# Optimization experiments

Measured on AMD Instinct MI355X. Metric: run time of the kernel, lower is better.

The kernel has to match this reference:

```python
import jax, jax.numpy as jnp
import numpy as np

B, S, D = 2, 2048, 3584
H, KV, HD = 28, 4, 128
N_REP = H // KV          # 7
MAX_S = 2048
SCALE = HD ** -0.5
ROPE_BASE = 1_000_000.0  # Qwen2 rope theta


def _rope_tables(max_s, hd, base):
    inv = 1.0 / (base ** (np.arange(0, hd, 2, dtype=np.float32) / hd))  # [hd/2]
    ang = np.arange(max_s, dtype=np.float32)[:, None] * inv[None, :]    # [S, hd/2]
    return jnp.asarray(np.cos(ang)), jnp.asarray(np.sin(ang))


def apply_rotary(x, cos, sin):
    # x: [b, s, h, hd] with interleaved complex pairs (torch view_as_complex layout)
    xr = x[..., 0::2]
    xi = x[..., 1::2]
    cos = cos[None, :, None, :]
    sin = sin[None, :, None, :]
    yr = xr * cos - xi * sin
    yi = xr * sin + xi * cos
    return jnp.stack([yr, yi], axis=-1).reshape(x.shape)


def setup_inputs() -> dict:
    key = jax.random.key(0)
    ks = jax.random.split(key, 8)
    w = 0.02
    x = jax.random.normal(ks[0], (B, S, D), jnp.float32)
    wq_w = jax.random.normal(ks[1], (H * HD, D), jnp.float32) * w
    wq_b = jax.random.normal(ks[2], (H * HD,), jnp.float32) * w
    wk_w = jax.random.normal(ks[3], (KV * HD, D), jnp.float32) * w
    wk_b = jax.random.normal(ks[4], (KV * HD,), jnp.float32) * w
    wv_w = jax.random.normal(ks[5], (KV * HD, D), jnp.float32) * w
    wv_b = jax.random.normal(ks[6], (KV * HD,), jnp.float32) * w
    wo_w = jax.random.normal(ks[7], (D, H * HD), jnp.float32) * w
    k_cache = jnp.zeros((B, MAX_S, KV, HD), jnp.float32)
    v_cache = jnp.zeros((B, MAX_S, KV, HD), jnp.float32)
    freqs_cos, freqs_sin = _rope_tables(MAX_S, HD, ROPE_BASE)
    # causal additive mask [s, t]; large-negative instead of -inf for safe grads
    mask = jnp.triu(jnp.full((S, S), -1e9, jnp.float32), k=1)
    return {"x": x, "wq_w": wq_w, "wq_b": wq_b, "wk_w": wk_w, "wk_b": wk_b,
            "wv_w": wv_w, "wv_b": wv_b, "wo_w": wo_w,
            "k_cache": k_cache, "v_cache": v_cache,
            "freqs_cos": freqs_cos, "freqs_sin": freqs_sin,
            "mask": mask, "start_pos": 0}


def reference(x, wq_w, wq_b, wk_w, wk_b, wv_w, wv_b, wo_w,
              k_cache, v_cache, freqs_cos, freqs_sin, mask, start_pos):
    bsz, seqlen, _ = x.shape
    end_pos = start_pos + seqlen
    q = (x @ wq_w.T + wq_b).reshape(bsz, seqlen, H, HD)
    k = (x @ wk_w.T + wk_b).reshape(bsz, seqlen, KV, HD)
    v = (x @ wv_w.T + wv_b).reshape(bsz, seqlen, KV, HD)
    cos = jax.lax.dynamic_slice_in_dim(freqs_cos, start_pos, seqlen, 0)
    sin = jax.lax.dynamic_slice_in_dim(freqs_sin, start_pos, seqlen, 0)
    q = apply_rotary(q, cos, sin)
    k = apply_rotary(k, cos, sin)
    # KV-cache write
    k_cache = jax.lax.dynamic_update_slice(k_cache, k, (0, start_pos, 0, 0))
    v_cache = jax.lax.dynamic_update_slice(v_cache, v, (0, start_pos, 0, 0))
    keys = k_cache[:bsz, :end_pos]    # [b, t, kv, hd]
    values = v_cache[:bsz, :end_pos]
    # GQA: repeat_interleave kv heads to n_heads
    keys = jnp.repeat(keys, N_REP, axis=2)      # [b, t, h, hd]
    values = jnp.repeat(values, N_REP, axis=2)
    scores = jnp.einsum('bshd,bthd->bsht', q, keys) * SCALE
    scores = scores + mask[None, :, None, :]
    probs = jax.nn.softmax(scores.astype(jnp.float32), axis=-1).astype(x.dtype)
    out = jnp.einsum('bsht,bthd->bshd', probs, values)
    out = out.reshape(bsz, seqlen, H * HD)
    return out @ wo_w.T
```

## Files before the change

### kernel.cpp

```cpp
#include <hip/hip_runtime.h>
#include <hip/hip_bf16.h>

typedef __attribute__((ext_vector_type(4)))  float  f32x4;
typedef __attribute__((ext_vector_type(16))) float  f32x16;
typedef __attribute__((ext_vector_type(8)))  __bf16 bf16x8;
typedef __attribute__((ext_vector_type(4)))  __bf16 bf16x4;
typedef __attribute__((ext_vector_type(4)))  unsigned int u32x4;

constexpr int S_LEN = 2048, DMODEL = 3584, NH = 28, NKV = 4, HD = 128, NREP = 7;
constexpr float SCALE_LOG2 = 0.1275174331f;

__device__ __forceinline__ unsigned int pack2(float a, float b) {
  unsigned short ua = __builtin_bit_cast(unsigned short, (__bf16)a);
  unsigned short ub = __builtin_bit_cast(unsigned short, (__bf16)b);
  return (unsigned int)ua | ((unsigned int)ub << 16);
}

__global__ void cvt5_kernel(const float* __restrict__ s0, const float* __restrict__ s1,
                            const float* __restrict__ s2, const float* __restrict__ s3,
                            const float* __restrict__ s4,
                            __bf16* __restrict__ d0, __bf16* __restrict__ d1,
                            __bf16* __restrict__ d2, __bf16* __restrict__ d3,
                            __bf16* __restrict__ d4,
                            int n0, int n1, int n2, int n3, int* __restrict__ ctr, int total) {
  if (blockIdx.x == 0 && threadIdx.x == 0) *ctr = 0;
  for (int i = blockIdx.x * blockDim.x + threadIdx.x; i < total; i += gridDim.x * blockDim.x) {
    const float* s; __bf16* d; int j = i;
    if (j < n0) { s = s0; d = d0; }
    else { j -= n0;
      if (j < n1) { s = s1; d = d1; }
      else { j -= n1;
        if (j < n2) { s = s2; d = d2; }
        else { j -= n2;
          if (j < n3) { s = s3; d = d3; }
          else { j -= n3; s = s4; d = d4; }
        }
      }
    }
    float4 v = reinterpret_cast<const float4*>(s)[j];
    bf16x4 o;
    o[0] = (__bf16)v.x; o[1] = (__bf16)v.y; o[2] = (__bf16)v.z; o[3] = (__bf16)v.w;
    reinterpret_cast<bf16x4*>(d)[j] = o;
  }
}

#define GLDS16(gsrc, ldst)                                                              \
  __builtin_amdgcn_global_load_lds((const __attribute__((address_space(1))) void*)(gsrc),\
                                   (__attribute__((address_space(3))) void*)(ldst), 16, 0, 0)

template <int MODE>
__global__ __launch_bounds__(512, 2) void gemm256(
    const __bf16* __restrict__ A, const __bf16* __restrict__ Bw,
    const float* __restrict__ bias, void* __restrict__ Cout,
    int M, int N, int K,
    const float* __restrict__ fcos, const float* __restrict__ fsin,
    const int* __restrict__ sp_ptr, float scale)
{
  extern __shared__ char smem[];
  const int tid = threadIdx.x;
  const int lane = tid & 63, wid = tid >> 6;
  const int wm = wid >> 2, wn = wid & 3;
  const int l15 = lane & 15, g = (lane >> 4) & 3;

  const int chunk = gridDim.x >> 3;
  const int wg = (blockIdx.x & 7) * chunk + (blockIdx.x >> 3);
  const int nbx = N >> 8;
  const int by = wg / nbx, bx = wg % nbx;
  const int row0 = by * 256, col0 = bx * 256;

  const int srL   = 16 * (tid >> 6) + ((tid >> 2) & 15);
  const int cperm = ((tid & 3) * 8) ^ (((tid >> 5) & 1) * 16);
  const __bf16* pA0 = A + (size_t)(row0 + srL) * K + cperm;
  const __bf16* pA1 = pA0 + (size_t)128 * K;
  const __bf16* pB0 = Bw + (size_t)(col0 + srL) * K + cperm;
  const __bf16* pB1 = pB0 + (size_t)128 * K;
  char* ldsA = smem + tid * 16;
  char* ldsB = smem + 65536 + tid * 16;

  const int sw = ((l15 >> 3) & 1) << 5;
  const int aoff = wm * 8192 + l15 * 64 + ((g * 16) ^ sw);
  const int boff = 65536 + wn * 4096 + l15 * 64 + ((g * 16) ^ sw);

  f32x4 acc[8][4] = {};
  const int nt = K >> 5;

#pragma unroll
  for (int pt = 0; pt < 3; pt++) {
    const size_t ko = (size_t)pt * 32;
    char* sA = ldsA + pt * 16384;
    char* sB = ldsB + pt * 16384;
    GLDS16(pA0 + ko, sA);
    GLDS16(pA1 + ko, sA + 8192);
    GLDS16(pB0 + ko, sB);
    GLDS16(pB1 + ko, sB + 8192);
  }
  asm volatile("s_waitcnt vmcnt(8)" ::: "memory");
  __builtin_amdgcn_s_barrier();
  __builtin_amdgcn_sched_barrier(0);

  for (int t = 0; t < nt; t++) {
    const int slot = (t & 3) * 16384;
    const char* sa = smem + slot + aoff;
    const char* sb = smem + slot + boff;
    bf16x8 a0[4], a1[4], bfv[4];

#pragma unroll
    for (int fn = 0; fn < 4; fn++)
      bfv[fn] = *reinterpret_cast<const bf16x8*>(sb + fn * 1024);
#pragma unroll
    for (int fm = 0; fm < 4; fm++)
      a0[fm] = *reinterpret_cast<const bf16x8*>(sa + fm * 1024);
#pragma unroll
    for (int fm = 0; fm < 4; fm++)
      a1[fm] = *reinterpret_cast<const bf16x8*>(sa + (4 + fm) * 1024);

    if (t + 3 < nt) {
      const size_t ko = (size_t)(t + 3) * 32;
      char* sA = ldsA + ((t + 3) & 3) * 16384;
      char* sB = ldsB + ((t + 3) & 3) * 16384;
      GLDS16(pA0 + ko, sA);
      GLDS16(pA1 + ko, sA + 8192);
      GLDS16(pB0 + ko, sB);
      GLDS16(pB1 + ko, sB + 8192);
    }

    asm volatile("s_waitcnt lgkmcnt(4)" ::: "memory");
    __builtin_amdgcn_sched_barrier(0);
    __builtin_amdgcn_s_setprio(1);
#pragma unroll
    for (int fn = 0; fn < 4; fn++)
#pragma unroll
      for (int fm = 0; fm < 4; fm++)
        acc[fm][fn] = __builtin_amdgcn_mfma_f32_16x16x32_bf16(a0[fm], bfv[fn], acc[fm][fn], 0, 0, 0);
    __builtin_amdgcn_s_setprio(0);

    asm volatile("s_waitcnt lgkmcnt(0)" ::: "memory");
    __builtin_amdgcn_sched_barrier(0);
    __builtin_amdgcn_s_setprio(1);
#pragma unroll
    for (int fn = 0; fn < 4; fn++)
#pragma unroll
      for (int fm = 0; fm < 4; fm++)
        acc[4 + fm][fn] = __builtin_amdgcn_mfma_f32_16x16x32_bf16(a1[fm], bfv[fn], acc[4 + fm][fn], 0, 0, 0);
    __builtin_amdgcn_s_setprio(0);

    if (t < nt - 3)       asm volatile("s_waitcnt vmcnt(8)" ::: "memory");
    else if (t == nt - 3) asm volatile("s_waitcnt vmcnt(4)" ::: "memory");
    else if (t == nt - 2) asm volatile("s_waitcnt vmcnt(0)" ::: "memory");
    __builtin_amdgcn_s_barrier();
    __builtin_amdgcn_sched_barrier(0);
  }

  if constexpr (MODE == 0) {
    float* C = (float*)Cout;
#pragma unroll
    for (int fm = 0; fm < 8; fm++) {
      const int row = row0 + wm * 128 + fm * 16 + 4 * g;
#pragma unroll
      for (int fn = 0; fn < 4; fn++) {
        const int col = col0 + wn * 64 + fn * 16 + l15;
#pragma unroll
        for (int r = 0; r < 4; r++)
          C[(size_t)(row + r) * N + col] = acc[fm][fn][r];
      }
    }
  } else {
    __bf16* C = (__bf16*)Cout;
    const int sp = sp_ptr[0];
    float bval[4];
#pragma unroll
    for (int fn = 0; fn < 4; fn++) bval[fn] = bias[col0 + wn * 64 + fn * 16 + l15];
#pragma unroll
    for (int fm = 0; fm < 8; fm++) {
#pragma unroll
      for (int fn = 0; fn < 4; fn++) {
        const int col = col0 + wn * 64 + fn * 16 + l15;
        const int i = (col & (HD - 1)) >> 1;
#pragma unroll
        for (int r = 0; r < 4; r++) {
          const int row = row0 + wm * 128 + fm * 16 + 4 * g + r;
          float y = acc[fm][fn][r] + bval[fn];
          float p = __shfl_xor(y, 1);
          const int spos = sp + (row & (S_LEN - 1));
          const float c = fcos[spos * (HD / 2) + i];
          const float sn = fsin[spos * (HD / 2) + i];
          y = (col & 1) ? (p * sn + y * c) : (y * c - p * sn);
          C[(size_t)row * N + col] = (__bf16)(y * scale);
        }
      }
    }
  }
}

__global__ __launch_bounds__(256) void gemm_kv(
    const __bf16* __restrict__ A,
    const __bf16* __restrict__ Wk, const float* __restrict__ bk, __bf16* __restrict__ Ko,
    const __bf16* __restrict__ Wv, const float* __restrict__ bv, __bf16* __restrict__ Vo,
    const float* __restrict__ fcos, const float* __restrict__ fsin,
    const int* __restrict__ sp_ptr)
{
  constexpr int N = 512, K = 3584;
  __shared__ __bf16 As[128 * 32];
  __shared__ __bf16 Bs[128 * 32];
  const int tid = threadIdx.x;
  const int lane = tid & 63, wid = tid >> 6;
  const int l15 = lane & 15, g = lane >> 4;
  const int wr = wid >> 1, wc = wid & 1;
  const bool isK = blockIdx.x < 4;
  const __bf16* Bw = isK ? Wk : Wv;
  const float* bias = isK ? bk : bv;
  __bf16* Cout = isK ? Ko : Vo;
  const int row0 = blockIdx.y * 128;
  const int col0 = (blockIdx.x & 3) * 128;

  f32x4 acc[4][4] = {};

  const int srow = tid >> 2;
  const int scol = (tid & 3) * 8;
  const __bf16* Ag0 = A + (size_t)(row0 + srow) * K + scol;
  const __bf16* Ag1 = Ag0 + (size_t)64 * K;
  const __bf16* Bg0 = Bw + (size_t)(col0 + srow) * K + scol;
  const __bf16* Bg1 = Bg0 + (size_t)64 * K;
  __bf16* As0 = As + tid * 8;
  __bf16* As1 = As + 2048 + tid * 8;
  __bf16* Bs0 = Bs + tid * 8;
  __bf16* Bs1 = Bs + 2048 + tid * 8;

  for (int k0 = 0; k0 < K; k0 += 32) {
    GLDS16(Ag0 + k0, As0);
    GLDS16(Ag1 + k0, As1);
    GLDS16(Bg0 + k0, Bs0);
    GLDS16(Bg1 + k0, Bs1);
    __syncthreads();
    bf16x8 af[4], bfr[4];
#pragma unroll
    for (int m = 0; m < 4; m++)
      af[m] = *reinterpret_cast<const bf16x8*>(As + (wr * 64 + m * 16 + l15) * 32 + g * 8);
#pragma unroll
    for (int n = 0; n < 4; n++)
      bfr[n] = *reinterpret_cast<const bf16x8*>(Bs + (wc * 64 + n * 16 + l15) * 32 + g * 8);
#pragma unroll
    for (int m = 0; m < 4; m++)
#pragma unroll
      for (int n = 0; n < 4; n++)
        acc[m][n] = __builtin_amdgcn_mfma_f32_16x16x32_bf16(af[m], bfr[n], acc[m][n], 0, 0, 0);
    __syncthreads();
  }

  const int sp = sp_ptr[0];
#pragma unroll
  for (int m = 0; m < 4; m++) {
#pragma unroll
    for (int n = 0; n < 4; n++) {
      const int col = col0 + wc * 64 + n * 16 + l15;
      const float bval = bias[col];
      f32x4 v = acc[m][n];
#pragma unroll
      for (int r = 0; r < 4; r++) {
        const int row = row0 + wr * 64 + m * 16 + 4 * g + r;
        float y = v[r] + bval;
        if (isK) {
          float p = __shfl_xor(y, 1);
          const int i = (col & (HD - 1)) >> 1;
          const int spos = sp + (row & (S_LEN - 1));
          const float c = fcos[spos * (HD / 2) + i];
          const float sn = fsin[spos * (HD / 2) + i];
          y = (col & 1) ? (p * sn + y * c) : (y * c - p * sn);
        }
        Cout[(size_t)row * N + col] = (__bf16)y;
      }
    }
  }
}

__global__ void vtrans_kernel(const __bf16* __restrict__ Vg, __bf16* __restrict__ Vt) {
  __shared__ __bf16 t[32][33];
  const int bkv = blockIdx.z;
  const int b = bkv >> 2, kv = bkv & 3;
  const int s0 = blockIdx.x * 32, h0 = blockIdx.y * 32;
  const int tid = threadIdx.x;
#pragma unroll
  for (int c = 0; c < 4; c++) {
    int idx = c * 256 + tid;
    int sr = idx >> 5, hc = idx & 31;
    t[sr][hc] = Vg[(((size_t)b * S_LEN + s0 + sr) * NKV + kv) * HD + h0 + hc];
  }
  __syncthreads();
#pragma unroll
  for (int c = 0; c < 4; c++) {
    int idx = c * 256 + tid;
    int hr = idx >> 5, sc = idx & 31;
    Vt[(((size_t)b * NKV + kv) * HD + h0 + hr) * S_LEN + s0 + sc] = t[sc][hr];
  }
}

__global__ __launch_bounds__(256, 2) void attn_kernel(
    const __bf16* __restrict__ Qb, const __bf16* __restrict__ Kb,
    const __bf16* __restrict__ Vt, __bf16* __restrict__ Ob, int* __restrict__ ctr)
{
  __shared__ __align__(16) char asmem[65536];
  __shared__ int jsh;

  const int tid = threadIdx.x, lane = tid & 63, wid = tid >> 6;
  const int l31 = lane & 31, hh = lane >> 5;

  const int trow = tid >> 4;
  const int kcol = (((tid & 15) * 16) ^ ((trow & 7) << 4)) >> 1;
  const int vrow = tid >> 3;
  const int vcol = (((tid & 7) * 16) ^ ((vrow & 7) << 4)) >> 1;

  constexpr int NITEMS = 16 * NH * 2;

  while (true) {
    if (tid == 0) jsh = atomicAdd(ctr, 1);
    __syncthreads();
    const int j = jsh;
    if (j >= NITEMS) break;

    const int qi = 15 - (j / 56);
    const int r56 = j % 56;
    const int h = r56 >> 1, b = r56 & 1;
    const int kvh = h / NREP;
    const int qw = qi * 128 + wid * 32;
    const int qg = qw + l31;

    const __bf16* Kbase = Kb + ((size_t)b * S_LEN * NKV + kvh) * HD;
    const __bf16* Vbase = Vt + ((size_t)b * NKV + kvh) * (size_t)HD * S_LEN;

    bf16x8 qf[8];
    {
      const __bf16* qp = Qb + (((size_t)b * S_LEN + qg) * NH + h) * HD + hh * 8;
#pragma unroll
      for (int c = 0; c < 8; c++) qf[c] = *reinterpret_cast<const bf16x8*>(qp + c * 16);
    }

    f32x16 o[4] = {};
    float mrun = -3.0e38f, lsum = 0.0f;

    const int ntiles = 2 * qi + 2;

#define STAGE(T, S)                                                                     \
    do {                                                                                \
      const int k0_ = (T) * 64;                                                         \
      char* Kd_ = asmem + (S) * 32768;                                                  \
      char* Vd_ = Kd_ + 16384;                                                          \
      _Pragma("unroll")                                                                 \
      for (int p = 0; p < 4; p++) {                                                     \
        GLDS16(Kbase + (size_t)(k0_ + p * 16 + trow) * (NKV * HD) + kcol,               \
               Kd_ + (p * 256 + tid) * 16);                                             \
        GLDS16(Vbase + (size_t)(p * 32 + vrow) * S_LEN + k0_ + vcol,                    \
               Vd_ + (p * 256 + tid) * 16);                                             \
      }                                                                                 \
    } while (0)

    STAGE(0, 0);

    for (int t = 0; t < ntiles; t++) {
      __syncthreads();
      if (t + 1 < ntiles) STAGE(t + 1, (t + 1) & 1);

      const char* Ksb = asmem + (t & 1) * 32768;
      const char* Vsb = Ksb + 16384;
      const int k0 = t * 64;

      f32x16 s0 = {}, s1 = {};
      {
        const char* kp0 = Ksb + l31 * 256;
        const char* kp1 = kp0 + 32 * 256;
        const int sw = (l31 & 7) << 4;
        __builtin_amdgcn_s_setprio(1);
#pragma unroll
        for (int c = 0; c < 8; c++) {
          const int cb = (c * 32 + hh * 16) ^ sw;
          bf16x8 kf0 = *reinterpret_cast<const bf16x8*>(kp0 + cb);
          s0 = __builtin_amdgcn_mfma_f32_32x32x16_bf16(kf0, qf[c], s0, 0, 0, 0);
          bf16x8 kf1 = *reinterpret_cast<const bf16x8*>(kp1 + cb);
          s1 = __builtin_amdgcn_mfma_f32_32x32x16_bf16(kf1, qf[c], s1, 0, 0, 0);
        }
        __builtin_amdgcn_s_setprio(0);
      }

      if (k0 + 63 > qw) {
#pragma unroll
        for (int r = 0; r < 16; r++) {
          const int kvo = k0 + ((r & 3) + 8 * (r >> 2)) + 4 * hh;
          if (kvo > qg)      s0[r] = -1.0e9f;
          if (kvo + 32 > qg) s1[r] = -1.0e9f;
        }
      }

      float pmax = -3.0e38f;
#pragma unroll
      for (int r = 0; r < 16; r++) { pmax = fmaxf(pmax, s0[r]); pmax = fmaxf(pmax, s1[r]); }
      pmax = fmaxf(pmax, __shfl_xor(pmax, 32));
      if (!__all(pmax <= mrun + 11.5f)) {
        const float mnew = fmaxf(mrun, pmax);
        const float fs = exp2f(mrun - mnew);
        lsum *= fs;
#pragma unroll
        for (int dt = 0; dt < 4; dt++) o[dt] *= fs;
        mrun = mnew;
      }
      float psum = 0.0f;
#pragma unroll
      for (int r = 0; r < 16; r++) {
        s0[r] = exp2f(s0[r] - mrun); psum += s0[r];
        s1[r] = exp2f(s1[r] - mrun); psum += s1[r];
      }
      lsum += psum;

      unsigned int pk[2][8], px[2][8];
#pragma unroll
      for (int jj = 0; jj < 8; jj++) {
        pk[0][jj] = pack2(s0[2 * jj], s0[2 * jj + 1]);
        pk[1][jj] = pack2(s1[2 * jj], s1[2 * jj + 1]);
      }
#pragma unroll
      for (int tt = 0; tt < 2; tt++)
#pragma unroll
        for (int jj = 0; jj < 8; jj++) px[tt][jj] = __shfl_xor(pk[tt][jj], 32);

      __builtin_amdgcn_s_setprio(1);
#pragma unroll
      for (int tt = 0; tt < 2; tt++) {
#pragma unroll
        for (int c2 = 0; c2 < 2; c2++) {
          u32x4 pb4;
          if (hh == 0)
            pb4 = (u32x4){pk[tt][4 * c2], pk[tt][4 * c2 + 1], px[tt][4 * c2], px[tt][4 * c2 + 1]};
          else
            pb4 = (u32x4){px[tt][4 * c2 + 2], px[tt][4 * c2 + 3], pk[tt][4 * c2 + 2], pk[tt][4 * c2 + 3]};
          bf16x8 pbf = __builtin_bit_cast(bf16x8, pb4);
          const int colb = tt * 64 + c2 * 32 + hh * 16;
#pragma unroll
          for (int dt = 0; dt < 4; dt++) {
            const int d = dt * 32 + l31;
            bf16x8 vf = *reinterpret_cast<const bf16x8*>(Vsb + d * 128 + (colb ^ ((d & 7) << 4)));
            o[dt] = __builtin_amdgcn_mfma_f32_32x32x16_bf16(vf, pbf, o[dt], 0, 0, 0);
          }
        }
      }
      __builtin_amdgcn_s_setprio(0);
    }
#undef STAGE

    lsum += __shfl_xor(lsum, 32);
    const float inv = 1.0f / lsum;
    char* my = asmem + wid * 8192;
#pragma unroll
    for (int dt = 0; dt < 4; dt++) {
#pragma unroll
      for (int jj = 0; jj < 8; jj++) {
        const int r = 2 * jj;
        const int d = dt * 32 + ((r & 3) + 8 * (r >> 2)) + 4 * hh;
        const unsigned int w = pack2(o[dt][r] * inv, o[dt][r + 1] * inv);
        *reinterpret_cast<unsigned int*>(my + ((l31 * 256 + d * 2) ^ ((l31 & 7) << 4))) = w;
      }
    }
#pragma unroll
    for (int jj = 0; jj < 8; jj++) {
      const int idx = jj * 64 + lane;
      const int row = idx >> 4, c16 = idx & 15;
      u32x4 val = *reinterpret_cast<u32x4*>(my + row * 256 + ((c16 * 16) ^ ((row & 7) << 4)));
      *reinterpret_cast<u32x4*>(Ob + (size_t)(b * S_LEN + qw + row) * (NH * HD) + h * HD + c16 * 8) = val;
    }
  }
}

extern "C" void kernel_launch(void* const* d_in, const int* in_sizes, int n_in,
                              void* d_out, int out_size, void* d_ws, size_t ws_size,
                              hipStream_t stream) {
  (void)in_sizes; (void)n_in; (void)out_size; (void)ws_size;
  const float* x    = (const float*)d_in[0];
  const float* wq_w = (const float*)d_in[1];
  const float* wq_b = (const float*)d_in[2];
  const float* wk_w = (const float*)d_in[3];
  const float* wk_b = (const float*)d_in[4];
  const float* wv_w = (const float*)d_in[5];
  const float* wv_b = (const float*)d_in[6];
  const float* wo_w = (const float*)d_in[7];
  const float* fcos = (const float*)d_in[10];
  const float* fsin = (const float*)d_in[11];
  const int*   spp  = (const int*)d_in[13];
  float* out = (float*)d_out;

  constexpr size_t XB_N = (size_t)4096 * 3584;
  constexpr size_t WQ_N = (size_t)3584 * 3584;
  constexpr size_t WK_N = (size_t)512 * 3584;
  constexpr size_t WO_N = (size_t)3584 * 3584;
  constexpr size_t KB_N = (size_t)4096 * 512;

  __bf16* xb  = (__bf16*)d_ws;
  __bf16* wqb = xb + XB_N;
  __bf16* wkb = wqb + WQ_N;
  __bf16* wvb = wkb + WK_N;
  __bf16* wob = wvb + WK_N;
  __bf16* Qb  = wob + WO_N;
  __bf16* Kb  = Qb + XB_N;
  __bf16* Vg  = Kb + KB_N;
  __bf16* Vt  = Vg + KB_N;
  int*    ctr = (int*)(Vt + KB_N);
  __bf16* Ob  = xb;

  constexpr int N0 = (int)(XB_N / 4), N1 = (int)(WQ_N / 4), N2 = (int)(WK_N / 4),
                N3 = (int)(WK_N / 4), N4 = (int)(WO_N / 4);
  constexpr int NTOT = N0 + N1 + N2 + N3 + N4;
  cvt5_kernel<<<2048, 256, 0, stream>>>(x, wq_w, wk_w, wv_w, wo_w,
                                        xb, wqb, wkb, wvb, wob,
                                        N0, N1, N2, N3, ctr, NTOT);

  gemm256<2><<<dim3(224), 512, 131072, stream>>>(xb, wqb, wq_b, Qb, 4096, 3584, 3584,
                                                 fcos, fsin, spp, SCALE_LOG2);
  gemm_kv<<<dim3(8, 32), 256, 0, stream>>>(xb, wkb, wk_b, Kb, wvb, wv_b, Vg,
                                           fcos, fsin, spp);
  vtrans_kernel<<<dim3(64, 4, 8), 256, 0, stream>>>(Vg, Vt);
  attn_kernel<<<dim3(512), 256, 0, stream>>>(Qb, Kb, Vt, Ob, ctr);
  gemm256<0><<<dim3(224), 512, 131072, stream>>>(Ob, wob, nullptr, out, 4096, 3584, 3584,
                                                 nullptr, nullptr, nullptr, 1.0f);
}
```

Baseline: 432.9 us.

## Restructure GEMM main loop into double-buffered 64-wide K tiles with phased loads

Replaces the 4-slot, 3-deep prefetch ring of 32-wide K tiles with a two-buffer scheme over 64-wide K tiles. Each iteration is split into four MFMA phases, and global-to-LDS loads for the next tile are interleaved between them. Barriers are placed around each MFMA phase in a ping-pong style. The aim is better overlap of loads with MFMA work and fewer loop iterations, at the cost of more barriers per iteration and a shallower prefetch distance.

```diff
diff --git a/kernel.cpp b/kernel.cpp
--- a/kernel.cpp
+++ b/kernel.cpp
@@ -74,82 +74,85 @@
   const __bf16* pA1 = pA0 + (size_t)128 * K;
   const __bf16* pB0 = Bw + (size_t)(col0 + srL) * K + cperm;
   const __bf16* pB1 = pB0 + (size_t)128 * K;
-  char* ldsA = smem + tid * 16;
-  char* ldsB = smem + 65536 + tid * 16;
-
-  const int sw = ((l15 >> 3) & 1) << 5;
-  const int aoff = wm * 8192 + l15 * 64 + ((g * 16) ^ sw);
-  const int boff = 65536 + wn * 4096 + l15 * 64 + ((g * 16) ^ sw);
+  char* lds = smem + tid * 16;
+
+  const int rdo = l15 * 64 + ((g * 16) ^ (((l15 >> 3) & 1) << 5));
+  const int abase = wm * 8192 + rdo;
+  const int bbase = 32768 + (wn >> 1) * 8192 + (wn & 1) * 4096 + rdo;
 
   f32x4 acc[8][4] = {};
-  const int nt = K >> 5;
-
-#pragma unroll
-  for (int pt = 0; pt < 3; pt++) {
-    const size_t ko = (size_t)pt * 32;
-    char* sA = ldsA + pt * 16384;
-    char* sB = ldsB + pt * 16384;
-    GLDS16(pA0 + ko, sA);
-    GLDS16(pA1 + ko, sA + 8192);
-    GLDS16(pB0 + ko, sB);
-    GLDS16(pB1 + ko, sB + 8192);
-  }
-  asm volatile("s_waitcnt vmcnt(8)" ::: "memory");
+  const int nt = K >> 6;
+
+  GLDS16(pA0,      lds);          GLDS16(pA1,      lds + 8192);
+  GLDS16(pB0,      lds + 32768);  GLDS16(pB1,      lds + 40960);
+  GLDS16(pA0 + 32, lds + 16384);  GLDS16(pA1 + 32, lds + 24576);
+  GLDS16(pB0 + 32, lds + 49152);  GLDS16(pB1 + 32, lds + 57344);
+  asm volatile("s_waitcnt vmcnt(4)" ::: "memory");
   __builtin_amdgcn_s_barrier();
   __builtin_amdgcn_sched_barrier(0);
 
+#define PHASE_MFMA(ACCROW)                                                              \
+  __builtin_amdgcn_s_barrier();                                                         \
+  asm volatile("s_waitcnt lgkmcnt(0)" ::: "memory");                                    \
+  __builtin_amdgcn_sched_barrier(0);                                                    \
+  __builtin_amdgcn_s_setprio(1);                                                        \
+  _Pragma("unroll")                                                                     \
+  for (int fn = 0; fn < 4; fn++)                                                        \
+    _Pragma("unroll")                                                                   \
+    for (int fm = 0; fm < 4; fm++)                                                      \
+      acc[ACCROW + fm][fn] =                                                            \
+          __builtin_amdgcn_mfma_f32_16x16x32_bf16(af[fm], bfv[fn], acc[ACCROW + fm][fn],\
+                                                  0, 0, 0);                             \
+  __builtin_amdgcn_s_setprio(0);                                                        \
+  __builtin_amdgcn_s_barrier();
+
   for (int t = 0; t < nt; t++) {
-    const int slot = (t & 3) * 16384;
-    const char* sa = smem + slot + aoff;
-    const char* sb = smem + slot + boff;
-    bf16x8 a0[4], a1[4], bfv[4];
+    const int bb = (t & 1) << 16;
+    const char* sab = smem + bb;
+    char* stg = lds + (((t + 1) & 1) << 16);
+    const bool st = (t + 1 < nt);
+    const size_t ko = (size_t)(t + 1) * 64;
+    bf16x8 af[4], bfv[4];
 
 #pragma unroll
     for (int fn = 0; fn < 4; fn++)
-      bfv[fn] = *reinterpret_cast<const bf16x8*>(sb + fn * 1024);
+      bfv[fn] = *reinterpret_cast<const bf16x8*>(sab + bbase + fn * 1024);
 #pragma unroll
     for (int fm = 0; fm < 4; fm++)
-      a0[fm] = *reinterpret_cast<const bf16x8*>(sa + fm * 1024);
+      af[fm] = *reinterpret_cast<const bf16x8*>(sab + abase + fm * 1024);
+    if (st) { GLDS16(pA0 + ko, stg); GLDS16(pA1 + ko, stg + 8192); }
+    PHASE_MFMA(0)
+
 #pragma unroll
     for (int fm = 0; fm < 4; fm++)
-      a1[fm] = *reinterpret_cast<const bf16x8*>(sa + (4 + fm) * 1024);
-
-    if (t + 3 < nt) {
-      const size_t ko = (size_t)(t + 3) * 32;
-      char* sA = ldsA + ((t + 3) & 3) * 16384;
-      char* sB = ldsB + ((t + 3) & 3) * 16384;
-      GLDS16(pA0 + ko, sA);
-      GLDS16(pA1 + ko, sA + 8192);
-      GLDS16(pB0 + ko, sB);
-      GLDS16(pB1 + ko, sB + 8192);
-    }
-
-    asm volatile("s_waitcnt lgkmcnt(4)" ::: "memory");
-    __builtin_amdgcn_sched_barrier(0);
-    __builtin_amdgcn_s_setprio(1);
+      af[fm] = *reinterpret_cast<const bf16x8*>(sab + abase + (4 + fm) * 1024);
+    if (st) {
+      GLDS16(pB0 + ko, stg + 32768); GLDS16(pB1 + ko, stg + 40960);
+      asm volatile("s_waitcnt vmcnt(4)" ::: "memory");
+    } else {
+      asm volatile("s_waitcnt vmcnt(0)" ::: "memory");
+    }
+    PHASE_MFMA(4)
+
 #pragma unroll
     for (int fn = 0; fn < 4; fn++)
-#pragma unroll
-      for (int fm = 0; fm < 4; fm++)
-        acc[fm][fn] = __builtin_amdgcn_mfma_f32_16x16x32_bf16(a0[fm], bfv[fn], acc[fm][fn], 0, 0, 0);
-    __builtin_amdgcn_s_setprio(0);
-
-    asm volatile("s_waitcnt lgkmcnt(0)" ::: "memory");
-    __builtin_amdgcn_sched_barrier(0);
-    __builtin_amdgcn_s_setprio(1);
-#pragma unroll
-    for (int fn = 0; fn < 4; fn++)
-#pragma unroll
-      for (int fm = 0; fm < 4; fm++)
-        acc[4 + fm][fn] = __builtin_amdgcn_mfma_f32_16x16x32_bf16(a1[fm], bfv[fn], acc[4 + fm][fn], 0, 0, 0);
-    __builtin_amdgcn_s_setprio(0);
-
-    if (t < nt - 3)       asm volatile("s_waitcnt vmcnt(8)" ::: "memory");
-    else if (t == nt - 3) asm volatile("s_waitcnt vmcnt(4)" ::: "memory");
-    else if (t == nt - 2) asm volatile("s_waitcnt vmcnt(0)" ::: "memory");
-    __builtin_amdgcn_s_barrier();
-    __builtin_amdgcn_sched_barrier(0);
-  }
+      bfv[fn] = *reinterpret_cast<const bf16x8*>(sab + bbase + 16384 + fn * 1024);
+#pragma unroll
+    for (int fm = 0; fm < 4; fm++)
+      af[fm] = *reinterpret_cast<const bf16x8*>(sab + abase + 16384 + fm * 1024);
+    if (st) { GLDS16(pA0 + ko + 32, stg + 16384); GLDS16(pA1 + ko + 32, stg + 24576); }
+    PHASE_MFMA(0)
+
+#pragma unroll
+    for (int fm = 0; fm < 4; fm++)
+      af[fm] = *reinterpret_cast<const bf16x8*>(sab + abase + 16384 + (4 + fm) * 1024);
+    if (st) {
+      GLDS16(pB0 + ko + 32, stg + 49152); GLDS16(pB1 + ko + 32, stg + 57344);
+      asm volatile("s_waitcnt vmcnt(4)" ::: "memory");
+    }
+    PHASE_MFMA(4)
+  }
+#undef PHASE_MFMA
 
   if constexpr (MODE == 0) {
     float* C = (float*)Cout;
```

After: 440.4 us. Within noise of the previous version (+1.7%).

## Fuse V transpose into KV GEMM, use static attention grid with single-buffered LDS

Applied to the files above, without the earlier changes.

The V projection epilogue now writes directly into the transposed [b,kv,d,s] layout, removing the separate transpose kernel and its intermediate buffer. The attention kernel drops the atomic work-queue persistent loop and launches one block per work item (896) in a snake-ordered mapping to balance causal work. LDS is halved to a single K/V stage so four blocks can share a CU, giving up double-buffered prefetch in favour of occupancy. The V epilogue stores 4-element strided chunks, which may be less coalesced.

```diff
diff --git a/kernel.cpp b/kernel.cpp
--- a/kernel.cpp
+++ b/kernel.cpp
@@ -22,8 +22,7 @@
                             __bf16* __restrict__ d0, __bf16* __restrict__ d1,
                             __bf16* __restrict__ d2, __bf16* __restrict__ d3,
                             __bf16* __restrict__ d4,
-                            int n0, int n1, int n2, int n3, int* __restrict__ ctr, int total) {
-  if (blockIdx.x == 0 && threadIdx.x == 0) *ctr = 0;
+                            int n0, int n1, int n2, int n3, int total) {
   for (int i = blockIdx.x * blockDim.x + threadIdx.x; i < total; i += gridDim.x * blockDim.x) {
     const float* s; __bf16* d; int j = i;
     if (j < n0) { s = s0; d = d0; }
@@ -195,7 +194,7 @@
 __global__ __launch_bounds__(256) void gemm_kv(
     const __bf16* __restrict__ A,
     const __bf16* __restrict__ Wk, const float* __restrict__ bk, __bf16* __restrict__ Ko,
-    const __bf16* __restrict__ Wv, const float* __restrict__ bv, __bf16* __restrict__ Vo,
+    const __bf16* __restrict__ Wv, const float* __restrict__ bv, __bf16* __restrict__ Vt,
     const float* __restrict__ fcos, const float* __restrict__ fsin,
     const int* __restrict__ sp_ptr)
 {
@@ -209,7 +208,6 @@
   const bool isK = blockIdx.x < 4;
   const __bf16* Bw = isK ? Wk : Wv;
   const float* bias = isK ? bk : bv;
-  __bf16* Cout = isK ? Ko : Vo;
   const int row0 = blockIdx.y * 128;
   const int col0 = (blockIdx.x & 3) * 128;
 
@@ -248,58 +246,53 @@
   }
 
   const int sp = sp_ptr[0];
-#pragma unroll
-  for (int m = 0; m < 4; m++) {
-#pragma unroll
-    for (int n = 0; n < 4; n++) {
-      const int col = col0 + wc * 64 + n * 16 + l15;
-      const float bval = bias[col];
-      f32x4 v = acc[m][n];
-#pragma unroll
-      for (int r = 0; r < 4; r++) {
-        const int row = row0 + wr * 64 + m * 16 + 4 * g + r;
-        float y = v[r] + bval;
-        if (isK) {
+  if (isK) {
+#pragma unroll
+    for (int m = 0; m < 4; m++) {
+#pragma unroll
+      for (int n = 0; n < 4; n++) {
+        const int col = col0 + wc * 64 + n * 16 + l15;
+        const float bval = bias[col];
+        f32x4 v = acc[m][n];
+#pragma unroll
+        for (int r = 0; r < 4; r++) {
+          const int row = row0 + wr * 64 + m * 16 + 4 * g + r;
+          float y = v[r] + bval;
           float p = __shfl_xor(y, 1);
           const int i = (col & (HD - 1)) >> 1;
           const int spos = sp + (row & (S_LEN - 1));
           const float c = fcos[spos * (HD / 2) + i];
           const float sn = fsin[spos * (HD / 2) + i];
           y = (col & 1) ? (p * sn + y * c) : (y * c - p * sn);
+          Ko[(size_t)row * N + col] = (__bf16)y;
         }
-        Cout[(size_t)row * N + col] = (__bf16)y;
+      }
+    }
+  } else {
+    const int b4kv = ((row0 >> 11) * 4) + (blockIdx.x & 3);
+    __bf16* vbase = Vt + ((size_t)b4kv << 18);
+#pragma unroll
+    for (int m = 0; m < 4; m++) {
+#pragma unroll
+      for (int n = 0; n < 4; n++) {
+        const int d = wc * 64 + n * 16 + l15;
+        const float bval = bias[col0 + d];
+        const int s0 = (row0 + wr * 64 + m * 16 + 4 * g) & (S_LEN - 1);
+        f32x4 v = acc[m][n];
+        bf16x4 o;
+#pragma unroll
+        for (int r = 0; r < 4; r++) o[r] = (__bf16)(v[r] + bval);
+        *reinterpret_cast<bf16x4*>(vbase + (size_t)d * S_LEN + s0) = o;
       }
     }
   }
 }
 
-__global__ void vtrans_kernel(const __bf16* __restrict__ Vg, __bf16* __restrict__ Vt) {
-  __shared__ __bf16 t[32][33];
-  const int bkv = blockIdx.z;
-  const int b = bkv >> 2, kv = bkv & 3;
-  const int s0 = blockIdx.x * 32, h0 = blockIdx.y * 32;
-  const int tid = threadIdx.x;
-#pragma unroll
-  for (int c = 0; c < 4; c++) {
-    int idx = c * 256 + tid;
-    int sr = idx >> 5, hc = idx & 31;
-    t[sr][hc] = Vg[(((size_t)b * S_LEN + s0 + sr) * NKV + kv) * HD + h0 + hc];
-  }
-  __syncthreads();
-#pragma unroll
-  for (int c = 0; c < 4; c++) {
-    int idx = c * 256 + tid;
-    int hr = idx >> 5, sc = idx & 31;
-    Vt[(((size_t)b * NKV + kv) * HD + h0 + hr) * S_LEN + s0 + sc] = t[sc][hr];
-  }
-}
-
-__global__ __launch_bounds__(256, 2) void attn_kernel(
+__global__ __launch_bounds__(256, 4) void attn_kernel(
     const __bf16* __restrict__ Qb, const __bf16* __restrict__ Kb,
-    const __bf16* __restrict__ Vt, __bf16* __restrict__ Ob, int* __restrict__ ctr)
+    const __bf16* __restrict__ Vt, __bf16* __restrict__ Ob)
 {
-  __shared__ __align__(16) char asmem[65536];
-  __shared__ int jsh;
+  __shared__ __align__(16) char asmem[32768];
 
   const int tid = threadIdx.x, lane = tid & 63, wid = tid >> 6;
   const int l31 = lane & 31, hh = lane >> 5;
@@ -309,161 +302,151 @@
   const int vrow = tid >> 3;
   const int vcol = (((tid & 7) * 16) ^ ((vrow & 7) << 4)) >> 1;
 
-  constexpr int NITEMS = 16 * NH * 2;
-
-  while (true) {
-    if (tid == 0) jsh = atomicAdd(ctr, 1);
+  const int bid = blockIdx.x;
+  const int rr = bid >> 8, pos = bid & 255;
+  const int j = (rr & 1) ? ((rr << 8) + ((rr == 3 ? 127 : 255) - pos)) : ((rr << 8) + pos);
+
+  const int qi = 15 - (j / 56);
+  const int r56 = j % 56;
+  const int h = r56 >> 1, b = r56 & 1;
+  const int kvh = h / NREP;
+  const int qw = qi * 128 + wid * 32;
+  const int qg = qw + l31;
+
+  const __bf16* Kbase = Kb + ((size_t)b * S_LEN * NKV + kvh) * HD;
+  const __bf16* Vbase = Vt + ((size_t)b * NKV + kvh) * (size_t)HD * S_LEN;
+
+  bf16x8 qf[8];
+  {
+    const __bf16* qp = Qb + (((size_t)b * S_LEN + qg) * NH + h) * HD + hh * 8;
+#pragma unroll
+    for (int c = 0; c < 8; c++) qf[c] = *reinterpret_cast<const bf16x8*>(qp + c * 16);
+  }
+
+  f32x16 o[4] = {};
+  float mrun = -3.0e38f, lsum = 0.0f;
+
+  const int ntiles = 2 * qi + 2;
+
+  for (int t = 0; t < ntiles; t++) {
     __syncthreads();
-    const int j = jsh;
-    if (j >= NITEMS) break;
-
-    const int qi = 15 - (j / 56);
-    const int r56 = j % 56;
-    const int h = r56 >> 1, b = r56 & 1;
-    const int kvh = h / NREP;
-    const int qw = qi * 128 + wid * 32;
-    const int qg = qw + l31;
-
-    const __bf16* Kbase = Kb + ((size_t)b * S_LEN * NKV + kvh) * HD;
-    const __bf16* Vbase = Vt + ((size_t)b * NKV + kvh) * (size_t)HD * S_LEN;
-
-    bf16x8 qf[8];
     {
-      const __bf16* qp = Qb + (((size_t)b * S_LEN + qg) * NH + h) * HD + hh * 8;
-#pragma unroll
-      for (int c = 0; c < 8; c++) qf[c] = *reinterpret_cast<const bf16x8*>(qp + c * 16);
-    }
-
-    f32x16 o[4] = {};
-    float mrun = -3.0e38f, lsum = 0.0f;
-
-    const int ntiles = 2 * qi + 2;
-
-#define STAGE(T, S)                                                                     \
-    do {                                                                                \
-      const int k0_ = (T) * 64;                                                         \
-      char* Kd_ = asmem + (S) * 32768;                                                  \
-      char* Vd_ = Kd_ + 16384;                                                          \
-      _Pragma("unroll")                                                                 \
-      for (int p = 0; p < 4; p++) {                                                     \
-        GLDS16(Kbase + (size_t)(k0_ + p * 16 + trow) * (NKV * HD) + kcol,               \
-               Kd_ + (p * 256 + tid) * 16);                                             \
-        GLDS16(Vbase + (size_t)(p * 32 + vrow) * S_LEN + k0_ + vcol,                    \
-               Vd_ + (p * 256 + tid) * 16);                                             \
-      }                                                                                 \
-    } while (0)
-
-    STAGE(0, 0);
-
-    for (int t = 0; t < ntiles; t++) {
-      __syncthreads();
-      if (t + 1 < ntiles) STAGE(t + 1, (t + 1) & 1);
-
-      const char* Ksb = asmem + (t & 1) * 32768;
-      const char* Vsb = Ksb + 16384;
-      const int k0 = t * 64;
-
-      f32x16 s0 = {}, s1 = {};
-      {
-        const char* kp0 = Ksb + l31 * 256;
-        const char* kp1 = kp0 + 32 * 256;
-        const int sw = (l31 & 7) << 4;
-        __builtin_amdgcn_s_setprio(1);
-#pragma unroll
-        for (int c = 0; c < 8; c++) {
-          const int cb = (c * 32 + hh * 16) ^ sw;
-          bf16x8 kf0 = *reinterpret_cast<const bf16x8*>(kp0 + cb);
-          s0 = __builtin_amdgcn_mfma_f32_32x32x16_bf16(kf0, qf[c], s0, 0, 0, 0);
-          bf16x8 kf1 = *reinterpret_cast<const bf16x8*>(kp1 + cb);
-          s1 = __builtin_amdgcn_mfma_f32_32x32x16_bf16(kf1, qf[c], s1, 0, 0, 0);
+      const int k0_ = t * 64;
+#pragma unroll
+      for (int p = 0; p < 4; p++) {
+        GLDS16(Kbase + (size_t)(k0_ + p * 16 + trow) * (NKV * HD) + kcol,
+               asmem + (p * 256 + tid) * 16);
+        GLDS16(Vbase + (size_t)(p * 32 + vrow) * S_LEN + k0_ + vcol,
+               asmem + 16384 + (p * 256 + tid) * 16);
+      }
+    }
+    __syncthreads();
+
+    const char* Ksb = asmem;
+    const char* Vsb = asmem + 16384;
+    const int k0 = t * 64;
+
+    f32x16 s0 = {}, s1 = {};
+    {
+      const char* kp0 = Ksb + l31 * 256;
+      const char* kp1 = kp0 + 32 * 256;
+      const int sw = (l31 & 7) << 4;
+      __builtin_amdgcn_s_setprio(1);
+#pragma unroll
+      for (int c = 0; c < 8; c++) {
+        const int cb = (c * 32 + hh * 16) ^ sw;
+        bf16x8 kf0 = *reinterpret_cast<const bf16x8*>(kp0 + cb);
+        s0 = __builtin_amdgcn_mfma_f32_32x32x16_bf16(kf0, qf[c], s0, 0, 0, 0);
+        bf16x8 kf1 = *reinterpret_cast<const bf16x8*>(kp1 + cb);
+        s1 = __builtin_amdgcn_mfma_f32_32x32x16_bf16(kf1, qf[c], s1, 0, 0, 0);
+      }
+      __builtin_amdgcn_s_setprio(0);
+    }
+
+    if (k0 + 63 > qw) {
+#pragma unroll
+      for (int r = 0; r < 16; r++) {
+        const int kvo = k0 + ((r & 3) + 8 * (r >> 2)) + 4 * hh;
+        if (kvo > qg)      s0[r] = -1.0e9f;
+        if (kvo + 32 > qg) s1[r] = -1.0e9f;
+      }
+    }
+
+    float pmax = -3.0e38f;
+#pragma unroll
+    for (int r = 0; r < 16; r++) { pmax = fmaxf(pmax, s0[r]); pmax = fmaxf(pmax, s1[r]); }
+    pmax = fmaxf(pmax, __shfl_xor(pmax, 32));
+    if (!__all(pmax <= mrun + 11.5f)) {
+      const float mnew = fmaxf(mrun, pmax);
+      const float fs = exp2f(mrun - mnew);
+      lsum *= fs;
+#pragma unroll
+      for (int dt = 0; dt < 4; dt++) o[dt] *= fs;
+      mrun = mnew;
+    }
+    float psum = 0.0f;
+#pragma unroll
+    for (int r = 0; r < 16; r++) {
+      s0[r] = exp2f(s0[r] - mrun); psum += s0[r];
+      s1[r] = exp2f(s1[r] - mrun); psum += s1[r];
+    }
+    lsum += psum;
+
+    unsigned int pk[2][8], px[2][8];
+#pragma unroll
+    for (int jj = 0; jj < 8; jj++) {
+      pk[0][jj] = pack2(s0[2 * jj], s0[2 * jj + 1]);
+      pk[1][jj] = pack2(s1[2 * jj], s1[2 * jj + 1]);
+    }
+#pragma unroll
+    for (int tt = 0; tt < 2; tt++)
+#pragma unroll
+      for (int jj = 0; jj < 8; jj++) px[tt][jj] = __shfl_xor(pk[tt][jj], 32);
+
+    __builtin_amdgcn_s_setprio(1);
+#pragma unroll
+    for (int tt = 0; tt < 2; tt++) {
+#pragma unroll
+      for (int c2 = 0; c2 < 2; c2++) {
+        u32x4 pb4;
+        if (hh == 0)
+          pb4 = (u32x4){pk[tt][4 * c2], pk[tt][4 * c2 + 1], px[tt][4 * c2], px[tt][4 * c2 + 1]};
+        else
+          pb4 = (u32x4){px[tt][4 * c2 + 2], px[tt][4 * c2 + 3], pk[tt][4 * c2 + 2], pk[tt][4 * c2 + 3]};
+        bf16x8 pbf = __builtin_bit_cast(bf16x8, pb4);
+        const int colb = tt * 64 + c2 * 32 + hh * 16;
+#pragma unroll
+        for (int dt = 0; dt < 4; dt++) {
+          const int d = dt * 32 + l31;
+          bf16x8 vf = *reinterpret_cast<const bf16x8*>(Vsb + d * 128 + (colb ^ ((d & 7) << 4)));
+          o[dt] = __builtin_amdgcn_mfma_f32_32x32x16_bf16(vf, pbf, o[dt], 0, 0, 0);
         }
-        __builtin_amdgcn_s_setprio(0);
-      }
-
-      if (k0 + 63 > qw) {
-#pragma unroll
-        for (int r = 0; r < 16; r++) {
-          const int kvo = k0 + ((r & 3) + 8 * (r >> 2)) + 4 * hh;
-          if (kvo > qg)      s0[r] = -1.0e9f;
-          if (kvo + 32 > qg) s1[r] = -1.0e9f;
-        }
-      }
-
-      float pmax = -3.0e38f;
-#pragma unroll
-      for (int r = 0; r < 16; r++) { pmax = fmaxf(pmax, s0[r]); pmax = fmaxf(pmax, s1[r]); }
-      pmax = fmaxf(pmax, __shfl_xor(pmax, 32));
-      if (!__all(pmax <= mrun + 11.5f)) {
-        const float mnew = fmaxf(mrun, pmax);
-        const float fs = exp2f(mrun - mnew);
-        lsum *= fs;
-#pragma unroll
-        for (int dt = 0; dt < 4; dt++) o[dt] *= fs;
-        mrun = mnew;
-      }
-      float psum = 0.0f;
-#pragma unroll
-      for (int r = 0; r < 16; r++) {
-        s0[r] = exp2f(s0[r] - mrun); psum += s0[r];
-        s1[r] = exp2f(s1[r] - mrun); psum += s1[r];
-      }
-      lsum += psum;
-
-      unsigned int pk[2][8], px[2][8];
-#pragma unroll
-      for (int jj = 0; jj < 8; jj++) {
-        pk[0][jj] = pack2(s0[2 * jj], s0[2 * jj + 1]);
-        pk[1][jj] = pack2(s1[2 * jj], s1[2 * jj + 1]);
-      }
-#pragma unroll
-      for (int tt = 0; tt < 2; tt++)
-#pragma unroll
-        for (int jj = 0; jj < 8; jj++) px[tt][jj] = __shfl_xor(pk[tt][jj], 32);
-
-      __builtin_amdgcn_s_setprio(1);
-#pragma unroll
-      for (int tt = 0; tt < 2; tt++) {
-#pragma unroll
-        for (int c2 = 0; c2 < 2; c2++) {
-          u32x4 pb4;
-          if (hh == 0)
-            pb4 = (u32x4){pk[tt][4 * c2], pk[tt][4 * c2 + 1], px[tt][4 * c2], px[tt][4 * c2 + 1]};
-          else
-            pb4 = (u32x4){px[tt][4 * c2 + 2], px[tt][4 * c2 + 3], pk[tt][4 * c2 + 2], pk[tt][4 * c2 + 3]};
-          bf16x8 pbf = __builtin_bit_cast(bf16x8, pb4);
-          const int colb = tt * 64 + c2 * 32 + hh * 16;
-#pragma unroll
-          for (int dt = 0; dt < 4; dt++) {
-            const int d = dt * 32 + l31;
-            bf16x8 vf = *reinterpret_cast<const bf16x8*>(Vsb + d * 128 + (colb ^ ((d & 7) << 4)));
-            o[dt] = __builtin_amdgcn_mfma_f32_32x32x16_bf16(vf, pbf, o[dt], 0, 0, 0);
-          }
-        }
-      }
-      __builtin_amdgcn_s_setprio(0);
-    }
-#undef STAGE
-
-    lsum += __shfl_xor(lsum, 32);
-    const float inv = 1.0f / lsum;
-    char* my = asmem + wid * 8192;
-#pragma unroll
-    for (int dt = 0; dt < 4; dt++) {
-#pragma unroll
-      for (int jj = 0; jj < 8; jj++) {
-        const int r = 2 * jj;
-        const int d = dt * 32 + ((r & 3) + 8 * (r >> 2)) + 4 * hh;
-        const unsigned int w = pack2(o[dt][r] * inv, o[dt][r + 1] * inv);
-        *reinterpret_cast<unsigned int*>(my + ((l31 * 256 + d * 2) ^ ((l31 & 7) << 4))) = w;
-      }
-    }
+      }
+    }
+    __builtin_amdgcn_s_setprio(0);
+  }
+
+  __syncthreads();
+
+  lsum += __shfl_xor(lsum, 32);
+  const float inv = 1.0f / lsum;
+  char* my = asmem + wid * 8192;
+#pragma unroll
+  for (int dt = 0; dt < 4; dt++) {
 #pragma unroll
     for (int jj = 0; jj < 8; jj++) {
-      const int idx = jj * 64 + lane;
-      const int row = idx >> 4, c16 = idx & 15;
-      u32x4 val = *reinterpret_cast<u32x4*>(my + row * 256 + ((c16 * 16) ^ ((row & 7) << 4)));
-      *reinterpret_cast<u32x4*>(Ob + (size_t)(b * S_LEN + qw + row) * (NH * HD) + h * HD + c16 * 8) = val;
-    }
+      const int r = 2 * jj;
+      const int d = dt * 32 + ((r & 3) + 8 * (r >> 2)) + 4 * hh;
+      const unsigned int w = pack2(o[dt][r] * inv, o[dt][r + 1] * inv);
+      *reinterpret_cast<unsigned int*>(my + ((l31 * 256 + d * 2) ^ ((l31 & 7) << 4))) = w;
+    }
+  }
+#pragma unroll
+  for (int jj = 0; jj < 8; jj++) {
+    const int idx = jj * 64 + lane;
+    const int row = idx >> 4, c16 = idx & 15;
+    u32x4 val = *reinterpret_cast<u32x4*>(my + row * 256 + ((c16 * 16) ^ ((row & 7) << 4)));
+    *reinterpret_cast<u32x4*>(Ob + (size_t)(b * S_LEN + qw + row) * (NH * HD) + h * HD + c16 * 8) = val;
   }
 }
 
@@ -497,9 +480,7 @@
   __bf16* wob = wvb + WK_N;
   __bf16* Qb  = wob + WO_N;
   __bf16* Kb  = Qb + XB_N;
-  __bf16* Vg  = Kb + KB_N;
-  __bf16* Vt  = Vg + KB_N;
-  int*    ctr = (int*)(Vt + KB_N);
+  __bf16* Vt  = Kb + KB_N;
   __bf16* Ob  = xb;
 
   constexpr int N0 = (int)(XB_N / 4), N1 = (int)(WQ_N / 4), N2 = (int)(WK_N / 4),
@@ -507,14 +488,13 @@
   constexpr int NTOT = N0 + N1 + N2 + N3 + N4;
   cvt5_kernel<<<2048, 256, 0, stream>>>(x, wq_w, wk_w, wv_w, wo_w,
                                         xb, wqb, wkb, wvb, wob,
-                                        N0, N1, N2, N3, ctr, NTOT);
+                                        N0, N1, N2, N3, NTOT);
 
   gemm256<2><<<dim3(224), 512, 131072, stream>>>(xb, wqb, wq_b, Qb, 4096, 3584, 3584,
                                                  fcos, fsin, spp, SCALE_LOG2);
-  gemm_kv<<<dim3(8, 32), 256, 0, stream>>>(xb, wkb, wk_b, Kb, wvb, wv_b, Vg,
+  gemm_kv<<<dim3(8, 32), 256, 0, stream>>>(xb, wkb, wk_b, Kb, wvb, wv_b, Vt,
                                            fcos, fsin, spp);
-  vtrans_kernel<<<dim3(64, 4, 8), 256, 0, stream>>>(Vg, Vt);
-  attn_kernel<<<dim3(512), 256, 0, stream>>>(Qb, Kb, Vt, Ob, ctr);
+  attn_kernel<<<dim3(896), 256, 0, stream>>>(Qb, Kb, Vt, Ob);
   gemm256<0><<<dim3(224), 512, 131072, stream>>>(Ob, wob, nullptr, out, 4096, 3584, 3584,
                                                  nullptr, nullptr, nullptr, 1.0f);
 }
```

After: 627.8 us. 45.0% more time.
